# Kernel tuning notes

Hardware: AMD Instinct MI355X
Metric: run time of the kernel (lower is better)

## Reference

```python
import jax, jax.numpy as jnp
import numpy as np
from jax import lax

B, S = 2, 1024
T = B * S
HIDDEN, Q_LORA_RANK = 7168, 1536
N_HEADS, HEAD_DIM, ROPE_DIM = 64, 128, 64
INDEX_TOPK = 2048
QUANT_BLOCK = 128
F8_MAX = 448.0  # float8_e4m3fn max
SOFTMAX_SCALE = HEAD_DIM ** -0.5


def quant_dequant_ue8m0(x):
    """Simulate per-128-block fp8(e4m3) quantization with ue8m0 (power-of-2, ceil) scales."""
    shp = x.shape
    xb = x.reshape(shp[:-1] + (shp[-1] // QUANT_BLOCK, QUANT_BLOCK))
    amax = jnp.max(jnp.abs(xb), axis=-1, keepdims=True)
    scale = jnp.exp2(jnp.ceil(jnp.log2(jnp.maximum(amax, 1e-4) / F8_MAX)))
    q = jnp.clip(xb / scale, -F8_MAX, F8_MAX).astype(jnp.float8_e4m3fn).astype(jnp.float32)
    return (q * scale).reshape(shp)


def rope_cos_sin(positions):
    half = ROPE_DIM // 2
    inv_freq = 1.0 / (10000.0 ** (jnp.arange(half, dtype=jnp.float32) * 2.0 / ROPE_DIM))
    ang = positions.astype(jnp.float32)[:, None] * inv_freq[None, :]  # [T, half]
    return jnp.cos(ang), jnp.sin(ang)


def apply_rope(x, cos, sin):
    half = x.shape[-1] // 2
    x1, x2 = x[..., :half], x[..., half:]
    return jnp.concatenate([x1 * cos - x2 * sin, x1 * sin + x2 * cos], axis=-1)


def setup_inputs() -> dict:
    key = jax.random.key(0)
    k0, k1, k2, k3, k4 = jax.random.split(key, 5)
    std = 0.02
    hidden_states = jax.random.normal(k0, (T, HIDDEN), jnp.float32)
    q_lora = jax.random.normal(k1, (T, Q_LORA_RANK), jnp.float32)
    wq_b = jax.random.normal(k2, (N_HEADS * HEAD_DIM, Q_LORA_RANK), jnp.float32) * std
    wk = jax.random.normal(k3, (HEAD_DIM, HIDDEN), jnp.float32) * std
    k_norm_w = jnp.ones((HEAD_DIM,), jnp.float32)
    k_norm_b = jnp.zeros((HEAD_DIM,), jnp.float32)
    w_proj = jax.random.normal(k4, (N_HEADS, HIDDEN), jnp.float32) * std
    positions = jnp.tile(jnp.arange(S, dtype=jnp.int32), B)  # local position within each sequence
    seq_lens = jnp.full((B,), S, dtype=jnp.int32)
    return {"hidden_states": hidden_states, "q_lora": q_lora, "wq_b": wq_b, "wk": wk,
            "k_norm_w": k_norm_w, "k_norm_b": k_norm_b, "w_proj": w_proj,
            "positions": positions, "seq_lens": seq_lens}


def reference(hidden_states, q_lora, wq_b, wk, k_norm_w, k_norm_b, w_proj, positions, seq_lens):
    # --- projections ---
    q = (q_lora @ wq_b.T).reshape(T, N_HEADS, HEAD_DIM)
    k = hidden_states @ wk.T  # [T, HEAD_DIM]
    # k_norm: LayerNorm(head_dim, eps=1e-6) in fp32
    mu = jnp.mean(k, axis=-1, keepdims=True)
    kc = k - mu
    k = kc * lax.rsqrt(jnp.mean(kc * kc, axis=-1, keepdims=True) + 1e-6) * k_norm_w + k_norm_b
    # --- RoPE on first ROPE_DIM dims of q (per head) and k ---
    cos, sin = rope_cos_sin(positions)
    q = jnp.concatenate([apply_rope(q[..., :ROPE_DIM], cos[:, None, :], sin[:, None, :]),
                         q[..., ROPE_DIM:]], axis=-1)
    k = jnp.concatenate([apply_rope(k[..., :ROPE_DIM], cos, sin), k[..., ROPE_DIM:]], axis=-1)
    # --- fp8 ue8m0 quant-dequant (simulates q_fp8 / per_token_quant_and_transform) ---
    q = quant_dequant_ue8m0(q)
    k = quant_dequant_ue8m0(k)
    # --- head weights (weights_proj, head-count and softmax scaling folded in) ---
    weights = (hidden_states @ w_proj.T) * (N_HEADS ** -0.5) * SOFTMAX_SCALE  # [T, H]
    # --- variable-length causal bounds (compute_cu_seqlen_kv_bounds_nocache) ---
    cu = jnp.concatenate([jnp.zeros((1,), jnp.int32), jnp.cumsum(seq_lens).astype(jnp.int32)])
    batch_ids = jnp.repeat(jnp.arange(seq_lens.shape[0], dtype=jnp.int32), seq_lens,
                           total_repeat_length=T)
    ks_ = cu[batch_ids]                                   # start of each token's KV window
    local_pos = jnp.arange(T, dtype=jnp.int32) - ks_
    ke_ = ks_ + local_pos + 1                             # exclusive end (causal)
    pos_n = jnp.arange(T, dtype=jnp.int32)
    mask = (pos_n[None, :] >= ks_[:, None]) & (pos_n[None, :] < ke_[:, None])  # [T, T]
    # --- fp8_mqa_logits: logits[m,n] = sum_h w[m,h] * relu(q[m,h] . k[n]) ---
    qh = jnp.transpose(q, (1, 0, 2))  # [H, T, D]
    wh = weights.T                    # [H, T]
    def step(acc, hw):
        qh_i, w_i = hw
        return acc + jax.nn.relu(qh_i @ k.T) * w_i[:, None], None
    logits, _ = lax.scan(step, jnp.zeros((T, T), jnp.float32), (qh, wh))
    logits = jnp.where(mask, logits, -jnp.inf)
    # --- top-k selection + local-index remap ---
    k_take = min(INDEX_TOPK, T)
    _, idx = lax.top_k(logits, k_take)
    local = idx - ks_[:, None]
    valid = (local >= 0) & (idx < ke_[:, None])
    topk_indices = jnp.where(valid, local, -1).astype(jnp.int32)
    return logits, topk_indices
```

## Files before the change

### kernel.cpp

```cpp
#include <hip/hip_runtime.h>
#include <math.h>
#include <stdint.h>

#define T_TOK 2048
#define HIDDEN 7168
#define RANK 1536
#define NH 64
#define HD 128
#define NQ (NH*HD)
#define RH 32
#define KSPLIT 8
#define KCHUNK (HIDDEN/KSPLIT)
#define NKW 192

#define MASK_VAL (-3.0e38f)

typedef short bf16x8 __attribute__((ext_vector_type(8)));
typedef float f32x4  __attribute__((ext_vector_type(4)));

#define GLL16(src, dst) __builtin_amdgcn_global_load_lds( \
    (const __attribute__((address_space(1))) void*)(src), \
    (__attribute__((address_space(3))) void*)(dst), 16, 0, 0)

__device__ __forceinline__ float qd_e4m3(float x){
  float ax = fabsf(x);
  float s = (x < 0.f) ? -1.f : 1.f;
  float q;
  if (ax < 0.015625f) {
    q = rintf(ax * 512.f) * 0.001953125f;
  } else {
    int e; (void)frexpf(ax, &e);
    float quant = ldexpf(1.f, e - 4);
    q = rintf(ax / quant) * quant;
  }
  return s * q;
}

__device__ __forceinline__ float ue8m0_scale(float amax){
  float y = fmaxf(amax, 1e-4f) / 448.f;
  int e; float m = frexpf(y, &e);
  int ce = (m == 0.5f) ? (e - 1) : e;
  return ldexpf(1.f, ce);
}

__device__ __forceinline__ unsigned short f2bf_rne(float x){
  unsigned int u = __float_as_uint(x);
  unsigned int r = u + 0x7FFFu + ((u >> 16) & 1u);
  return (unsigned short)(r >> 16);
}

__device__ __forceinline__ void split_bf16(float x, unsigned short& hi, unsigned short& lo){
  unsigned int u = __float_as_uint(x);
  hi = (unsigned short)(u >> 16);
  float xh = __uint_as_float(u & 0xFFFF0000u);
  lo = f2bf_rne(x - xh);
}

__global__ void kt_cossin(const int* __restrict__ pos, float* __restrict__ cost,
                          float* __restrict__ sint){
  int idx = blockIdx.x*256 + threadIdx.x;
  if (idx >= T_TOK*RH) return;
  int t = idx >> 5, j = idx & 31;
  float ex = (float)(2*j) / 64.0f;
  float p10 = (float)pow(10000.0, (double)ex);
  float invf = 1.0f / p10;
  float ang = (float)pos[t] * invf;
  cost[idx] = (float)cos((double)ang);
  sint[idx] = (float)sin((double)ang);
}

__global__ __launch_bounds__(256) void kw_split(const float* __restrict__ Wk,
                                                const float* __restrict__ Wp,
                                                unsigned short* __restrict__ Bh,
                                                unsigned short* __restrict__ Bl){
  int idx = blockIdx.x*256 + threadIdx.x;
  int e0 = idx*8;
  if (e0 >= NKW*HIDDEN) return;
  int n = e0 / HIDDEN, k = e0 - n*HIDDEN;
  const float* src = (n < HD) ? (Wk + (size_t)n*HIDDEN + k) : (Wp + (size_t)(n-HD)*HIDDEN + k);
  float4 a0 = *(const float4*)src;
  float4 a1 = *(const float4*)(src+4);
  float f[8] = {a0.x,a0.y,a0.z,a0.w,a1.x,a1.y,a1.z,a1.w};
  unsigned short h[8], l[8];
  #pragma unroll
  for (int i=0;i<8;i++) split_bf16(f[i], h[i], l[i]);
  *(uint4*)(Bh + e0) = *(const uint4*)h;
  *(uint4*)(Bl + e0) = *(const uint4*)l;
}

__global__ __launch_bounds__(256) void kb3(const float* __restrict__ H,
                                           const unsigned short* __restrict__ Bhg,
                                           const unsigned short* __restrict__ Blg,
                                           float* __restrict__ P){
  __shared__ unsigned short Ah[64*32], Al[64*32], Bh[NKW*32], Bl[NKW*32];
  int ks = blockIdx.x, m0 = blockIdx.y*64, k0 = ks*KCHUNK;
  int tid = threadIdx.x, lane = tid & 63;
  int w = tid >> 6, wr = w >> 1, wc = w & 1;
  int ar = tid >> 2, ac = (tid & 3)*8;
  const float* Arow = H + (size_t)(m0+ar)*HIDDEN + k0 + ac;
  int awb = (ar*64 + ac*2) ^ (((ar>>1)&3)<<4);
  f32x4 acc[2][6];
  #pragma unroll
  for (int i=0;i<2;i++)
    #pragma unroll
    for (int j=0;j<6;j++)
      #pragma unroll
      for (int r=0;r<4;r++) acc[i][j][r] = 0.f;

  for (int kb = 0; kb < KCHUNK; kb += 32){
    float4 a0 = *(const float4*)(Arow + kb);
    float4 a1 = *(const float4*)(Arow + kb + 4);
    __syncthreads();
    {
      float f[8] = {a0.x,a0.y,a0.z,a0.w,a1.x,a1.y,a1.z,a1.w};
      unsigned short h[8], l[8];
      #pragma unroll
      for (int i=0;i<8;i++) split_bf16(f[i], h[i], l[i]);
      *(uint4*)((char*)Ah + awb) = *(const uint4*)h;
      *(uint4*)((char*)Al + awb) = *(const uint4*)l;
    }
    #pragma unroll
    for (int i=0;i<3;i++){
      int ch = w + 4*i;
      int o = ch*1024 + lane*16;
      int row = o >> 6;
      int cb = (o & 63) ^ (((row>>1)&3)<<4);
      size_t srcoff = (size_t)row*HIDDEN + k0 + kb + (cb>>1);
      GLL16(Bhg + srcoff, (char*)Bh + ch*1024);
      GLL16(Blg + srcoff, (char*)Bl + ch*1024);
    }
    __syncthreads();
    bf16x8 ah[2], alr[2], bh[6], bl[6];
    #pragma unroll
    for (int mf=0;mf<2;mf++){
      int rl = wr*32 + mf*16 + (lane&15);
      int ad = (rl*64 + ((lane>>4)*16)) ^ (((rl>>1)&3)<<4);
      ah[mf]  = *(const bf16x8*)((const char*)Ah + ad);
      alr[mf] = *(const bf16x8*)((const char*)Al + ad);
    }
    #pragma unroll
    for (int nf=0;nf<6;nf++){
      int jl = wc*96 + nf*16 + (lane&15);
      int ad = (jl*64 + ((lane>>4)*16)) ^ (((jl>>1)&3)<<4);
      bh[nf] = *(const bf16x8*)((const char*)Bh + ad);
      bl[nf] = *(const bf16x8*)((const char*)Bl + ad);
    }
    #pragma unroll
    for (int mf=0;mf<2;mf++)
      #pragma unroll
      for (int nf=0;nf<6;nf++){
        acc[mf][nf] = __builtin_amdgcn_mfma_f32_16x16x32_bf16(ah[mf],  bh[nf], acc[mf][nf], 0,0,0);
        acc[mf][nf] = __builtin_amdgcn_mfma_f32_16x16x32_bf16(alr[mf], bh[nf], acc[mf][nf], 0,0,0);
        acc[mf][nf] = __builtin_amdgcn_mfma_f32_16x16x32_bf16(ah[mf],  bl[nf], acc[mf][nf], 0,0,0);
      }
  }
  #pragma unroll
  for (int mf=0;mf<2;mf++)
    #pragma unroll
    for (int r=0;r<4;r++){
      int t = m0 + wr*32 + mf*16 + (lane>>4)*4 + r;
      #pragma unroll
      for (int nf=0;nf<6;nf++){
        int n = wc*96 + nf*16 + (lane&15);
        P[((size_t)ks*T_TOK + t)*NKW + n] = acc[mf][nf][r];
      }
    }
}

__global__ __launch_bounds__(128) void kc2(const float* __restrict__ P,
                                           const float* __restrict__ knw,
                                           const float* __restrict__ knb,
                                           const float* __restrict__ cost,
                                           const float* __restrict__ sint,
                                           unsigned short* __restrict__ k16,
                                           float* __restrict__ abuf){
  __shared__ float sh[128];
  __shared__ float red[128];
  int t = blockIdx.x, d = threadIdx.x;
  float v = 0.f;
  #pragma unroll
  for (int s=0;s<KSPLIT;s++) v += P[((size_t)s*T_TOK + t)*NKW + d];
  if (d < NH){
    float wv = 0.f;
    #pragma unroll
    for (int s=0;s<KSPLIT;s++) wv += P[((size_t)s*T_TOK + t)*NKW + HD + d];
    wv = wv * 0.125f;
    wv = wv * 0.08838834764831845f;
    abuf[(size_t)t*NH + d] = wv;
  }
  red[d] = v; __syncthreads();
  for (int s=64;s>0;s>>=1){ if (d<s) red[d] += red[d+s]; __syncthreads(); }
  float mu = red[0] * (1.0f/128.0f); __syncthreads();
  float kc = v - mu;
  red[d] = kc*kc; __syncthreads();
  for (int s=64;s>0;s>>=1){ if (d<s) red[d] += red[d+s]; __syncthreads(); }
  float var = red[0] * (1.0f/128.0f); __syncthreads();
  float rs = 1.0f / sqrtf(var + 1e-6f);
  float nv = ((kc * rs) * knw[d]) + knb[d];
  sh[d] = nv; __syncthreads();
  float rv;
  if (d < RH)            rv = sh[d]*cost[t*RH + d]      - sh[d+RH]*sint[t*RH + d];
  else if (d < 2*RH)     rv = sh[d-RH]*sint[t*RH + d-RH] + sh[d]*cost[t*RH + d-RH];
  else                   rv = nv;
  red[d] = fabsf(rv); __syncthreads();
  for (int s=64;s>0;s>>=1){ if (d<s) red[d] = fmaxf(red[d], red[d+s]); __syncthreads(); }
  float scale = ue8m0_scale(red[0]);
  k16[(size_t)t*HD + d] = f2bf_rne(qd_e4m3(rv / scale) * scale);
}

__global__ __launch_bounds__(256,2) void ka2(const float* __restrict__ A,
                                             const float* __restrict__ B,
                                             const float* __restrict__ cost,
                                             const float* __restrict__ sint,
                                             unsigned short* __restrict__ q16){
  __shared__ unsigned short Ah[128*32], Al[128*32], Bh[128*32], Bl[128*32];
  __shared__ float amx[128][2];
  int n0 = blockIdx.x*128, m0 = blockIdx.y*128;
  int tid = threadIdx.x, lane = tid & 63;
  int w = tid >> 6, wr = w >> 1, wc = w & 1;
  int row = tid >> 1, half = tid & 1;
  const float* Arow = A + (size_t)(m0+row)*RANK + half*16;
  const float* Brow = B + (size_t)(n0+row)*RANK + half*16;
  int sw = ((row >> 1) & 3) << 4;
  int wb0 = row*64 + half*32;
  f32x4 acc[4][4];
  #pragma unroll
  for (int i=0;i<4;i++)
    #pragma unroll
    for (int j=0;j<4;j++)
      #pragma unroll
      for (int r=0;r<4;r++) acc[i][j][r] = 0.f;

  for (int kb = 0; kb < RANK; kb += 32){
    float4 av4[4], bv4[4];
    #pragma unroll
    for (int c=0;c<4;c++) av4[c] = *(const float4*)(Arow + kb + 4*c);
    #pragma unroll
    for (int c=0;c<4;c++) bv4[c] = *(const float4*)(Brow + kb + 4*c);
    __syncthreads();
    {
      unsigned short h[16], l[16];
      const float* f = (const float*)av4;
      #pragma unroll
      for (int i=0;i<16;i++) split_bf16(f[i], h[i], l[i]);
      *(uint4*)((char*)Ah + ((wb0   )^sw)) = *(const uint4*)&h[0];
      *(uint4*)((char*)Ah + ((wb0+16)^sw)) = *(const uint4*)&h[8];
      *(uint4*)((char*)Al + ((wb0   )^sw)) = *(const uint4*)&l[0];
      *(uint4*)((char*)Al + ((wb0+16)^sw)) = *(const uint4*)&l[8];
      const float* g = (const float*)bv4;
      #pragma unroll
      for (int i=0;i<16;i++) split_bf16(g[i], h[i], l[i]);
      *(uint4*)((char*)Bh + ((wb0   )^sw)) = *(const uint4*)&h[0];
      *(uint4*)((char*)Bh + ((wb0+16)^sw)) = *(const uint4*)&h[8];
      *(uint4*)((char*)Bl + ((wb0   )^sw)) = *(const uint4*)&l[0];
      *(uint4*)((char*)Bl + ((wb0+16)^sw)) = *(const uint4*)&l[8];
    }
    __syncthreads();
    bf16x8 ah[4], bh[4], tmp[4];
    #pragma unroll
    for (int mf=0;mf<4;mf++){
      int rl = wr*64 + mf*16 + (lane&15);
      int ad = (rl*64 + ((lane>>4)*16)) ^ ((((rl>>1)&3))<<4);
      ah[mf] = *(const bf16x8*)((const char*)Ah + ad);
    }
    #pragma unroll
    for (int nf=0;nf<4;nf++){
      int rl = wc*64 + nf*16 + (lane&15);
      int ad = (rl*64 + ((lane>>4)*16)) ^ ((((rl>>1)&3))<<4);
      bh[nf] = *(const bf16x8*)((const char*)Bh + ad);
    }
    #pragma unroll
    for (int mf=0;mf<4;mf++)
      #pragma unroll
      for (int nf=0;nf<4;nf++)
        acc[mf][nf] = __builtin_amdgcn_mfma_f32_16x16x32_bf16(ah[mf], bh[nf], acc[mf][nf], 0,0,0);
    #pragma unroll
    for (int mf=0;mf<4;mf++){
      int rl = wr*64 + mf*16 + (lane&15);
      int ad = (rl*64 + ((lane>>4)*16)) ^ ((((rl>>1)&3))<<4);
      tmp[mf] = *(const bf16x8*)((const char*)Al + ad);
    }
    #pragma unroll
    for (int mf=0;mf<4;mf++)
      #pragma unroll
      for (int nf=0;nf<4;nf++)
        acc[mf][nf] = __builtin_amdgcn_mfma_f32_16x16x32_bf16(tmp[mf], bh[nf], acc[mf][nf], 0,0,0);
    #pragma unroll
    for (int nf=0;nf<4;nf++){
      int rl = wc*64 + nf*16 + (lane&15);
      int ad = (rl*64 + ((lane>>4)*16)) ^ ((((rl>>1)&3))<<4);
      tmp[nf] = *(const bf16x8*)((const char*)Bl + ad);
    }
    #pragma unroll
    for (int mf=0;mf<4;mf++)
      #pragma unroll
      for (int nf=0;nf<4;nf++)
        acc[mf][nf] = __builtin_amdgcn_mfma_f32_16x16x32_bf16(ah[mf], tmp[nf], acc[mf][nf], 0,0,0);
  }

  if (wc == 0){
    #pragma unroll
    for (int mf=0;mf<4;mf++)
      #pragma unroll
      for (int r=0;r<4;r++){
        int t = m0 + wr*64 + mf*16 + (lane>>4)*4 + r;
        #pragma unroll
        for (int nf=0;nf<2;nf++){
          int d0 = nf*16 + (lane&15);
          float c = cost[t*RH + d0], s = sint[t*RH + d0];
          float x1 = acc[mf][nf][r], x2 = acc[mf][nf+2][r];
          acc[mf][nf][r]   = __fsub_rn(__fmul_rn(x1,c), __fmul_rn(x2,s));
          acc[mf][nf+2][r] = __fadd_rn(__fmul_rn(x1,s), __fmul_rn(x2,c));
        }
      }
  }
  float pm[16];
  #pragma unroll
  for (int mf=0;mf<4;mf++)
    #pragma unroll
    for (int r=0;r<4;r++){
      float m1 = fmaxf(fabsf(acc[mf][0][r]), fabsf(acc[mf][1][r]));
      float m2 = fmaxf(fabsf(acc[mf][2][r]), fabsf(acc[mf][3][r]));
      pm[mf*4+r] = fmaxf(m1, m2);
    }
  #pragma unroll
  for (int msk=1; msk<16; msk<<=1)
    #pragma unroll
    for (int i=0;i<16;i++) pm[i] = fmaxf(pm[i], __shfl_xor(pm[i], msk, 16));
  if ((lane & 15) == 0){
    #pragma unroll
    for (int mf=0;mf<4;mf++)
      #pragma unroll
      for (int r=0;r<4;r++)
        amx[wr*64 + mf*16 + (lane>>4)*4 + r][wc] = pm[mf*4+r];
  }
  __syncthreads();
  #pragma unroll
  for (int mf=0;mf<4;mf++)
    #pragma unroll
    for (int r=0;r<4;r++){
      int rl = wr*64 + mf*16 + (lane>>4)*4 + r;
      int t = m0 + rl;
      float scl = ue8m0_scale(fmaxf(amx[rl][0], amx[rl][1]));
      #pragma unroll
      for (int nf=0;nf<4;nf++){
        float v = acc[mf][nf][r];
        float qv = qd_e4m3(v / scl) * scl;
        q16[(size_t)t*NQ + n0 + wc*64 + nf*16 + (lane&15)] = f2bf_rne(qv);
      }
    }
}

__global__ __launch_bounds__(256,2) void ke2(const unsigned short* __restrict__ q16,
                                             const unsigned short* __restrict__ k16,
                                             const float* __restrict__ W,
                                             const int* __restrict__ seq,
                                             float* __restrict__ out){
  __shared__ unsigned short Kt[128*128];
  __shared__ unsigned short Qt[2][64*128];
  __shared__ float Wl[64*64];
  int j0 = blockIdx.x*128, t0 = blockIdx.y*64;
  int tid = threadIdx.x;
  int s0 = seq[0];
  int ks0 = (t0 < s0) ? 0 : s0;
  if (j0 > t0 + 63 || j0 + 127 < ks0){
    int tl = tid >> 2, c0 = (tid & 3) * 32;
    float4 m4 = make_float4(MASK_VAL, MASK_VAL, MASK_VAL, MASK_VAL);
    float* rowp = out + (size_t)(t0+tl)*T_TOK + j0 + c0;
    #pragma unroll
    for (int c=0;c<32;c+=4) *(float4*)(rowp + c) = m4;
    return;
  }
  int lane = tid & 63, w = tid >> 6, wt = w >> 1, wj = w & 1;
  #pragma unroll
  for (int is=0; is<8; ++is){
    int o = is*4096 + w*1024 + lane*16;
    int row = o >> 8;
    int os = o ^ ((row & 7) << 4);
    int col = (os & 255) >> 1;
    GLL16(k16 + (size_t)(j0 + row)*HD + col, (char*)Kt + is*4096 + w*1024);
  }
  {
    int tl = tid >> 2, h0 = (tid & 3) * 16;
    float wv[16];
    #pragma unroll
    for (int c=0;c<4;c++) *(float4*)&wv[4*c] = *(const float4*)(W + (size_t)(t0+tl)*NH + h0 + 4*c);
    #pragma unroll
    for (int i=0;i<16;i++) Wl[(h0+i)*64 + tl] = wv[i];
  }
  #pragma unroll
  for (int is=0; is<4; ++is){
    int o = is*4096 + w*1024 + lane*16;
    int row = o >> 8;
    int os = o ^ ((row & 7) << 4);
    int col = (os & 255) >> 1;
    GLL16(q16 + (size_t)(t0 + row)*NQ + 0*HD + col, (char*)&Qt[0][0] + is*4096 + w*1024);
  }
  __syncthreads();
  bf16x8 bk[4][4];
  #pragma unroll
  for (int jf=0;jf<4;jf++){
    int jl = wj*64 + jf*16 + (lane&15);
    int sz = (jl & 7) << 4;
    #pragma unroll
    for (int kf=0;kf<4;kf++)
      bk[jf][kf] = *(const bf16x8*)((const char*)Kt + ((jl*256 + kf*64 + ((lane>>4)*16)) ^ sz));
  }
  bool skip = (j0 + wj*64 > t0 + wt*32 + 31) || (j0 + wj*64 + 63 < ks0);
  f32x4 acc[2][4];
  #pragma unroll
  for (int a=0;a<2;a++)
    #pragma unroll
    for (int b=0;b<4;b++)
      #pragma unroll
      for (int r=0;r<4;r++) acc[a][b][r] = 0.f;

  for (int h = 0; h < NH; ++h){
    if (h < NH-1){
      char* dst = (char*)&Qt[(h+1)&1][0];
      #pragma unroll
      for (int is=0; is<4; ++is){
        int o = is*4096 + w*1024 + lane*16;
        int row = o >> 8;
        int os = o ^ ((row & 7) << 4);
        int col = (os & 255) >> 1;
        GLL16(q16 + (size_t)(t0 + row)*NQ + (size_t)(h+1)*HD + col, dst + is*4096 + w*1024);
      }
    }
    if (!skip){
      const char* qb = (const char*)&Qt[h&1][0];
      bf16x8 aq[2][4];
      #pragma unroll
      for (int tf=0;tf<2;tf++){
        int tl = wt*32 + tf*16 + (lane&15);
        int sz = (tl & 7) << 4;
        #pragma unroll
        for (int kf=0;kf<4;kf++)
          aq[tf][kf] = *(const bf16x8*)(qb + ((tl*256 + kf*64 + ((lane>>4)*16)) ^ sz));
      }
      f32x4 pp[2][4];
      #pragma unroll
      for (int a=0;a<2;a++)
        #pragma unroll
        for (int b=0;b<4;b++)
          #pragma unroll
          for (int r=0;r<4;r++) pp[a][b][r] = 0.f;
      #pragma unroll
      for (int kf=0;kf<4;kf++)
        #pragma unroll
        for (int tf=0;tf<2;tf++)
          #pragma unroll
          for (int jf=0;jf<4;jf++)
            pp[tf][jf] = __builtin_amdgcn_mfma_f32_16x16x32_bf16(aq[tf][kf], bk[jf][kf], pp[tf][jf], 0,0,0);
      #pragma unroll
      for (int tf=0;tf<2;tf++)
        #pragma unroll
        for (int r=0;r<4;r++){
          float wv = Wl[h*64 + wt*32 + tf*16 + (lane>>4)*4 + r];
          #pragma unroll
          for (int jf=0;jf<4;jf++)
            acc[tf][jf][r] = fmaf(wv, fmaxf(pp[tf][jf][r], 0.f), acc[tf][jf][r]);
        }
    }
    __syncthreads();
  }
  #pragma unroll
  for (int tf=0;tf<2;tf++)
    #pragma unroll
    for (int r=0;r<4;r++){
      int t = t0 + wt*32 + tf*16 + (lane>>4)*4 + r;
      #pragma unroll
      for (int jf=0;jf<4;jf++){
        int j = j0 + wj*64 + jf*16 + (lane&15);
        bool ok = (j >= ks0) && (j <= t);
        out[(size_t)t*T_TOK + j] = ok ? acc[tf][jf][r] : MASK_VAL;
      }
    }
}

__global__ __launch_bounds__(256) void kf_topk(const float* __restrict__ logits,
                                               const int* __restrict__ seq,
                                               float* __restrict__ outIdx){
  __shared__ unsigned long long keys[1024];
  int t = blockIdx.x, tid = threadIdx.x;
  int s0 = seq[0];
  int ks = (t < s0) ? 0 : s0;
  int nv = t - ks + 1;
  for (int i = tid; i < 1024; i += 256){
    unsigned long long key = 0ull;
    if (i < nv){
      float v = logits[(size_t)t*T_TOK + ks + i];
      unsigned int b = __float_as_uint(v);
      unsigned int ov = (b & 0x80000000u) ? ~b : (b | 0x80000000u);
      key = ((unsigned long long)ov << 32) | (unsigned long long)(0x7FFFFFFFu - (unsigned)i);
    }
    keys[i] = key;
  }
  for (int size = 2; size <= 1024; size <<= 1){
    for (int stride = size >> 1; stride > 0; stride >>= 1){
      __syncthreads();
      for (int i = tid; i < 1024; i += 256){
        int p = i ^ stride;
        if (p > i){
          bool up = (i & size) == 0;
          unsigned long long a = keys[i], b2 = keys[p];
          if (up ? (a < b2) : (a > b2)){ keys[i] = b2; keys[p] = a; }
        }
      }
    }
  }
  __syncthreads();
  for (int p = tid; p < T_TOK; p += 256){
    float o = -1.0f;
    if (p < nv){
      unsigned int low = (unsigned int)(keys[p] & 0xFFFFFFFFull);
      o = (float)(int)(0x7FFFFFFFu - low);
    }
    outIdx[(size_t)t*T_TOK + p] = o;
  }
}

extern "C" void kernel_launch(void* const* d_in, const int* in_sizes, int n_in,
                              void* d_out, int out_size, void* d_ws, size_t ws_size,
                              hipStream_t stream){
  const float* hidden  = (const float*)d_in[0];
  const float* q_lora  = (const float*)d_in[1];
  const float* wq_b    = (const float*)d_in[2];
  const float* wk      = (const float*)d_in[3];
  const float* knw     = (const float*)d_in[4];
  const float* knb     = (const float*)d_in[5];
  const float* wproj   = (const float*)d_in[6];
  const int* positions = (const int*)d_in[7];
  const int* seq       = (const int*)d_in[8];

  char* ws = (char*)d_ws;
  unsigned short* q16 = (unsigned short*)ws;              ws += (size_t)T_TOK*NQ*2;
  float* P = (float*)ws;                                  ws += (size_t)KSPLIT*T_TOK*NKW*4;
  unsigned short* Whg = (unsigned short*)ws;              ws += (size_t)NKW*HIDDEN*2;
  unsigned short* Wlg = (unsigned short*)ws;              ws += (size_t)NKW*HIDDEN*2;
  unsigned short* k16 = (unsigned short*)ws;              ws += (size_t)T_TOK*HD*2;
  float* abuf = (float*)ws;                               ws += (size_t)T_TOK*NH*4;
  float* cost = (float*)ws;                               ws += (size_t)T_TOK*RH*4;
  float* sint = (float*)ws;                               ws += (size_t)T_TOK*RH*4;

  float* logits = (float*)d_out;
  float* topk   = logits + (size_t)T_TOK*T_TOK;

  kt_cossin<<<(T_TOK*RH)/256, 256, 0, stream>>>(positions, cost, sint);
  kw_split <<<(NKW*HIDDEN/8 + 255)/256, 256, 0, stream>>>(wk, wproj, Whg, Wlg);
  kb3      <<<dim3(KSPLIT, T_TOK/64), 256, 0, stream>>>(hidden, Whg, Wlg, P);
  kc2      <<<T_TOK, 128, 0, stream>>>(P, knw, knb, cost, sint, k16, abuf);
  ka2      <<<dim3(NQ/128, T_TOK/128), 256, 0, stream>>>(q_lora, wq_b, cost, sint, q16);
  ke2      <<<dim3(T_TOK/128, T_TOK/64), 256, 0, stream>>>(q16, k16, abuf, seq, logits);
  kf_topk  <<<T_TOK, 256, 0, stream>>>(logits, seq, topk);
}
```

Baseline: 348.8 us.

## Merge Q and K/weight projection GEMMs into one heterogeneous launch

```diff
diff --git a/kernel.cpp b/kernel.cpp
--- a/kernel.cpp
+++ b/kernel.cpp
@@ -88,83 +88,236 @@
   *(uint4*)(Bl + e0) = *(const uint4*)l;
 }
 
-__global__ __launch_bounds__(256) void kb3(const float* __restrict__ H,
-                                           const unsigned short* __restrict__ Bhg,
-                                           const unsigned short* __restrict__ Blg,
-                                           float* __restrict__ P){
-  __shared__ unsigned short Ah[64*32], Al[64*32], Bh[NKW*32], Bl[NKW*32];
-  int ks = blockIdx.x, m0 = blockIdx.y*64, k0 = ks*KCHUNK;
+__global__ __launch_bounds__(256,2) void kfat(const float* __restrict__ A,
+                                              const float* __restrict__ B,
+                                              const float* __restrict__ cost,
+                                              const float* __restrict__ sint,
+                                              unsigned short* __restrict__ q16,
+                                              const float* __restrict__ H,
+                                              const unsigned short* __restrict__ Bhg,
+                                              const unsigned short* __restrict__ Blg,
+                                              float* __restrict__ P){
+  __shared__ char smem[33792] __attribute__((aligned(16)));
+  int bid = blockIdx.x;
   int tid = threadIdx.x, lane = tid & 63;
-  int w = tid >> 6, wr = w >> 1, wc = w & 1;
-  int ar = tid >> 2, ac = (tid & 3)*8;
-  const float* Arow = H + (size_t)(m0+ar)*HIDDEN + k0 + ac;
-  int awb = (ar*64 + ac*2) ^ (((ar>>1)&3)<<4);
-  f32x4 acc[2][6];
-  #pragma unroll
-  for (int i=0;i<2;i++)
-    #pragma unroll
-    for (int j=0;j<6;j++)
-      #pragma unroll
-      for (int r=0;r<4;r++) acc[i][j][r] = 0.f;
-
-  for (int kb = 0; kb < KCHUNK; kb += 32){
-    float4 a0 = *(const float4*)(Arow + kb);
-    float4 a1 = *(const float4*)(Arow + kb + 4);
+
+  if (bid < 1024){
+    unsigned short* Ah = (unsigned short*)smem;
+    unsigned short* Al = Ah + 128*32;
+    unsigned short* Bh = Al + 128*32;
+    unsigned short* Bl = Bh + 128*32;
+    float (*amx)[2] = (float(*)[2])(smem + 32768);
+    int n0 = (bid & 63)*128, m0 = (bid >> 6)*128;
+    int w = tid >> 6, wr = w >> 1, wc = w & 1;
+    int row = tid >> 1, half = tid & 1;
+    const float* Arow = A + (size_t)(m0+row)*RANK + half*16;
+    const float* Brow = B + (size_t)(n0+row)*RANK + half*16;
+    int sw = ((row >> 1) & 3) << 4;
+    int wb0 = row*64 + half*32;
+    f32x4 acc[4][4];
+    #pragma unroll
+    for (int i=0;i<4;i++)
+      #pragma unroll
+      for (int j=0;j<4;j++)
+        #pragma unroll
+        for (int r=0;r<4;r++) acc[i][j][r] = 0.f;
+
+    for (int kb = 0; kb < RANK; kb += 32){
+      float4 av4[4], bv4[4];
+      #pragma unroll
+      for (int c=0;c<4;c++) av4[c] = *(const float4*)(Arow + kb + 4*c);
+      #pragma unroll
+      for (int c=0;c<4;c++) bv4[c] = *(const float4*)(Brow + kb + 4*c);
+      __syncthreads();
+      {
+        unsigned short h[16], l[16];
+        const float* f = (const float*)av4;
+        #pragma unroll
+        for (int i=0;i<16;i++) split_bf16(f[i], h[i], l[i]);
+        *(uint4*)((char*)Ah + ((wb0   )^sw)) = *(const uint4*)&h[0];
+        *(uint4*)((char*)Ah + ((wb0+16)^sw)) = *(const uint4*)&h[8];
+        *(uint4*)((char*)Al + ((wb0   )^sw)) = *(const uint4*)&l[0];
+        *(uint4*)((char*)Al + ((wb0+16)^sw)) = *(const uint4*)&l[8];
+        const float* g = (const float*)bv4;
+        #pragma unroll
+        for (int i=0;i<16;i++) split_bf16(g[i], h[i], l[i]);
+        *(uint4*)((char*)Bh + ((wb0   )^sw)) = *(const uint4*)&h[0];
+        *(uint4*)((char*)Bh + ((wb0+16)^sw)) = *(const uint4*)&h[8];
+        *(uint4*)((char*)Bl + ((wb0   )^sw)) = *(const uint4*)&l[0];
+        *(uint4*)((char*)Bl + ((wb0+16)^sw)) = *(const uint4*)&l[8];
+      }
+      __syncthreads();
+      bf16x8 ah[4], bh[4], tmp[4];
+      #pragma unroll
+      for (int mf=0;mf<4;mf++){
+        int rl = wr*64 + mf*16 + (lane&15);
+        int ad = (rl*64 + ((lane>>4)*16)) ^ ((((rl>>1)&3))<<4);
+        ah[mf] = *(const bf16x8*)((const char*)Ah + ad);
+      }
+      #pragma unroll
+      for (int nf=0;nf<4;nf++){
+        int rl = wc*64 + nf*16 + (lane&15);
+        int ad = (rl*64 + ((lane>>4)*16)) ^ ((((rl>>1)&3))<<4);
+        bh[nf] = *(const bf16x8*)((const char*)Bh + ad);
+      }
+      #pragma unroll
+      for (int mf=0;mf<4;mf++)
+        #pragma unroll
+        for (int nf=0;nf<4;nf++)
+          acc[mf][nf] = __builtin_amdgcn_mfma_f32_16x16x32_bf16(ah[mf], bh[nf], acc[mf][nf], 0,0,0);
+      #pragma unroll
+      for (int mf=0;mf<4;mf++){
+        int rl = wr*64 + mf*16 + (lane&15);
+        int ad = (rl*64 + ((lane>>4)*16)) ^ ((((rl>>1)&3))<<4);
+        tmp[mf] = *(const bf16x8*)((const char*)Al + ad);
+      }
+      #pragma unroll
+      for (int mf=0;mf<4;mf++)
+        #pragma unroll
+        for (int nf=0;nf<4;nf++)
+          acc[mf][nf] = __builtin_amdgcn_mfma_f32_16x16x32_bf16(tmp[mf], bh[nf], acc[mf][nf], 0,0,0);
+      #pragma unroll
+      for (int nf=0;nf<4;nf++){
+        int rl = wc*64 + nf*16 + (lane&15);
+        int ad = (rl*64 + ((lane>>4)*16)) ^ ((((rl>>1)&3))<<4);
+        tmp[nf] = *(const bf16x8*)((const char*)Bl + ad);
+      }
+      #pragma unroll
+      for (int mf=0;mf<4;mf++)
+        #pragma unroll
+        for (int nf=0;nf<4;nf++)
+          acc[mf][nf] = __builtin_amdgcn_mfma_f32_16x16x32_bf16(ah[mf], tmp[nf], acc[mf][nf], 0,0,0);
+    }
+
+    if (wc == 0){
+      #pragma unroll
+      for (int mf=0;mf<4;mf++)
+        #pragma unroll
+        for (int r=0;r<4;r++){
+          int t = m0 + wr*64 + mf*16 + (lane>>4)*4 + r;
+          #pragma unroll
+          for (int nf=0;nf<2;nf++){
+            int d0 = nf*16 + (lane&15);
+            float c = cost[t*RH + d0], s = sint[t*RH + d0];
+            float x1 = acc[mf][nf][r], x2 = acc[mf][nf+2][r];
+            acc[mf][nf][r]   = __fsub_rn(__fmul_rn(x1,c), __fmul_rn(x2,s));
+            acc[mf][nf+2][r] = __fadd_rn(__fmul_rn(x1,s), __fmul_rn(x2,c));
+          }
+        }
+    }
+    float pm[16];
+    #pragma unroll
+    for (int mf=0;mf<4;mf++)
+      #pragma unroll
+      for (int r=0;r<4;r++){
+        float m1 = fmaxf(fabsf(acc[mf][0][r]), fabsf(acc[mf][1][r]));
+        float m2 = fmaxf(fabsf(acc[mf][2][r]), fabsf(acc[mf][3][r]));
+        pm[mf*4+r] = fmaxf(m1, m2);
+      }
+    #pragma unroll
+    for (int msk=1; msk<16; msk<<=1)
+      #pragma unroll
+      for (int i=0;i<16;i++) pm[i] = fmaxf(pm[i], __shfl_xor(pm[i], msk, 16));
+    if ((lane & 15) == 0){
+      #pragma unroll
+      for (int mf=0;mf<4;mf++)
+        #pragma unroll
+        for (int r=0;r<4;r++)
+          amx[wr*64 + mf*16 + (lane>>4)*4 + r][wc] = pm[mf*4+r];
+    }
     __syncthreads();
-    {
-      float f[8] = {a0.x,a0.y,a0.z,a0.w,a1.x,a1.y,a1.z,a1.w};
-      unsigned short h[8], l[8];
-      #pragma unroll
-      for (int i=0;i<8;i++) split_bf16(f[i], h[i], l[i]);
-      *(uint4*)((char*)Ah + awb) = *(const uint4*)h;
-      *(uint4*)((char*)Al + awb) = *(const uint4*)l;
-    }
-    #pragma unroll
-    for (int i=0;i<3;i++){
-      int ch = w + 4*i;
-      int o = ch*1024 + lane*16;
-      int row = o >> 6;
-      int cb = (o & 63) ^ (((row>>1)&3)<<4);
-      size_t srcoff = (size_t)row*HIDDEN + k0 + kb + (cb>>1);
-      GLL16(Bhg + srcoff, (char*)Bh + ch*1024);
-      GLL16(Blg + srcoff, (char*)Bl + ch*1024);
-    }
-    __syncthreads();
-    bf16x8 ah[2], alr[2], bh[6], bl[6];
-    #pragma unroll
-    for (int mf=0;mf<2;mf++){
-      int rl = wr*32 + mf*16 + (lane&15);
-      int ad = (rl*64 + ((lane>>4)*16)) ^ (((rl>>1)&3)<<4);
-      ah[mf]  = *(const bf16x8*)((const char*)Ah + ad);
-      alr[mf] = *(const bf16x8*)((const char*)Al + ad);
-    }
-    #pragma unroll
-    for (int nf=0;nf<6;nf++){
-      int jl = wc*96 + nf*16 + (lane&15);
-      int ad = (jl*64 + ((lane>>4)*16)) ^ (((jl>>1)&3)<<4);
-      bh[nf] = *(const bf16x8*)((const char*)Bh + ad);
-      bl[nf] = *(const bf16x8*)((const char*)Bl + ad);
+    #pragma unroll
+    for (int mf=0;mf<4;mf++)
+      #pragma unroll
+      for (int r=0;r<4;r++){
+        int rl = wr*64 + mf*16 + (lane>>4)*4 + r;
+        int t = m0 + rl;
+        float scl = ue8m0_scale(fmaxf(amx[rl][0], amx[rl][1]));
+        #pragma unroll
+        for (int nf=0;nf<4;nf++){
+          float v = acc[mf][nf][r];
+          float qv = qd_e4m3(v / scl) * scl;
+          q16[(size_t)t*NQ + n0 + wc*64 + nf*16 + (lane&15)] = f2bf_rne(qv);
+        }
+      }
+  } else {
+    unsigned short* Ah = (unsigned short*)smem;
+    unsigned short* Al = Ah + 64*32;
+    unsigned short* Bh = Al + 64*32;
+    unsigned short* Bl = Bh + NKW*32;
+    int b2 = bid - 1024;
+    int ks = b2 & 7, m0 = (b2 >> 3)*64, k0 = ks*KCHUNK;
+    int w = tid >> 6, wr = w >> 1, wc = w & 1;
+    int ar = tid >> 2, ac = (tid & 3)*8;
+    const float* Arow = H + (size_t)(m0+ar)*HIDDEN + k0 + ac;
+    int awb = (ar*64 + ac*2) ^ (((ar>>1)&3)<<4);
+    f32x4 acc[2][6];
+    #pragma unroll
+    for (int i=0;i<2;i++)
+      #pragma unroll
+      for (int j=0;j<6;j++)
+        #pragma unroll
+        for (int r=0;r<4;r++) acc[i][j][r] = 0.f;
+
+    for (int kb = 0; kb < KCHUNK; kb += 32){
+      float4 a0 = *(const float4*)(Arow + kb);
+      float4 a1 = *(const float4*)(Arow + kb + 4);
+      __syncthreads();
+      {
+        float f[8] = {a0.x,a0.y,a0.z,a0.w,a1.x,a1.y,a1.z,a1.w};
+        unsigned short h[8], l[8];
+        #pragma unroll
+        for (int i=0;i<8;i++) split_bf16(f[i], h[i], l[i]);
+        *(uint4*)((char*)Ah + awb) = *(const uint4*)h;
+        *(uint4*)((char*)Al + awb) = *(const uint4*)l;
+      }
+      #pragma unroll
+      for (int i=0;i<3;i++){
+        int ch = w + 4*i;
+        int o = ch*1024 + lane*16;
+        int row = o >> 6;
+        int cb = (o & 63) ^ (((row>>1)&3)<<4);
+        size_t srcoff = (size_t)row*HIDDEN + k0 + kb + (cb>>1);
+        GLL16(Bhg + srcoff, (char*)Bh + ch*1024);
+        GLL16(Blg + srcoff, (char*)Bl + ch*1024);
+      }
+      __syncthreads();
+      bf16x8 ah[2], alr[2], bh[6], bl[6];
+      #pragma unroll
+      for (int mf=0;mf<2;mf++){
+        int rl = wr*32 + mf*16 + (lane&15);
+        int ad = (rl*64 + ((lane>>4)*16)) ^ (((rl>>1)&3)<<4);
+        ah[mf]  = *(const bf16x8*)((const char*)Ah + ad);
+        alr[mf] = *(const bf16x8*)((const char*)Al + ad);
+      }
+      #pragma unroll
+      for (int nf=0;nf<6;nf++){
+        int jl = wc*96 + nf*16 + (lane&15);
+        int ad = (jl*64 + ((lane>>4)*16)) ^ (((jl>>1)&3)<<4);
+        bh[nf] = *(const bf16x8*)((const char*)Bh + ad);
+        bl[nf] = *(const bf16x8*)((const char*)Bl + ad);
+      }
+      #pragma unroll
+      for (int mf=0;mf<2;mf++)
+        #pragma unroll
+        for (int nf=0;nf<6;nf++){
+          acc[mf][nf] = __builtin_amdgcn_mfma_f32_16x16x32_bf16(ah[mf],  bh[nf], acc[mf][nf], 0,0,0);
+          acc[mf][nf] = __builtin_amdgcn_mfma_f32_16x16x32_bf16(alr[mf], bh[nf], acc[mf][nf], 0,0,0);
+          acc[mf][nf] = __builtin_amdgcn_mfma_f32_16x16x32_bf16(ah[mf],  bl[nf], acc[mf][nf], 0,0,0);
+        }
     }
     #pragma unroll
     for (int mf=0;mf<2;mf++)
       #pragma unroll
-      for (int nf=0;nf<6;nf++){
-        acc[mf][nf] = __builtin_amdgcn_mfma_f32_16x16x32_bf16(ah[mf],  bh[nf], acc[mf][nf], 0,0,0);
-        acc[mf][nf] = __builtin_amdgcn_mfma_f32_16x16x32_bf16(alr[mf], bh[nf], acc[mf][nf], 0,0,0);
-        acc[mf][nf] = __builtin_amdgcn_mfma_f32_16x16x32_bf16(ah[mf],  bl[nf], acc[mf][nf], 0,0,0);
-      }
-  }
-  #pragma unroll
-  for (int mf=0;mf<2;mf++)
-    #pragma unroll
-    for (int r=0;r<4;r++){
-      int t = m0 + wr*32 + mf*16 + (lane>>4)*4 + r;
-      #pragma unroll
-      for (int nf=0;nf<6;nf++){
-        int n = wc*96 + nf*16 + (lane&15);
-        P[((size_t)ks*T_TOK + t)*NKW + n] = acc[mf][nf][r];
-      }
-    }
+      for (int r=0;r<4;r++){
+        int t = m0 + wr*32 + mf*16 + (lane>>4)*4 + r;
+        #pragma unroll
+        for (int nf=0;nf<6;nf++){
+          int n = wc*96 + nf*16 + (lane&15);
+          P[((size_t)ks*T_TOK + t)*NKW + n] = acc[mf][nf][r];
+        }
+      }
+  }
 }
 
 __global__ __launch_bounds__(128) void kc2(const float* __restrict__ P,
@@ -208,149 +361,6 @@
   k16[(size_t)t*HD + d] = f2bf_rne(qd_e4m3(rv / scale) * scale);
 }
 
-__global__ __launch_bounds__(256,2) void ka2(const float* __restrict__ A,
-                                             const float* __restrict__ B,
-                                             const float* __restrict__ cost,
-                                             const float* __restrict__ sint,
-                                             unsigned short* __restrict__ q16){
-  __shared__ unsigned short Ah[128*32], Al[128*32], Bh[128*32], Bl[128*32];
-  __shared__ float amx[128][2];
-  int n0 = blockIdx.x*128, m0 = blockIdx.y*128;
-  int tid = threadIdx.x, lane = tid & 63;
-  int w = tid >> 6, wr = w >> 1, wc = w & 1;
-  int row = tid >> 1, half = tid & 1;
-  const float* Arow = A + (size_t)(m0+row)*RANK + half*16;
-  const float* Brow = B + (size_t)(n0+row)*RANK + half*16;
-  int sw = ((row >> 1) & 3) << 4;
-  int wb0 = row*64 + half*32;
-  f32x4 acc[4][4];
-  #pragma unroll
-  for (int i=0;i<4;i++)
-    #pragma unroll
-    for (int j=0;j<4;j++)
-      #pragma unroll
-      for (int r=0;r<4;r++) acc[i][j][r] = 0.f;
-
-  for (int kb = 0; kb < RANK; kb += 32){
-    float4 av4[4], bv4[4];
-    #pragma unroll
-    for (int c=0;c<4;c++) av4[c] = *(const float4*)(Arow + kb + 4*c);
-    #pragma unroll
-    for (int c=0;c<4;c++) bv4[c] = *(const float4*)(Brow + kb + 4*c);
-    __syncthreads();
-    {
-      unsigned short h[16], l[16];
-      const float* f = (const float*)av4;
-      #pragma unroll
-      for (int i=0;i<16;i++) split_bf16(f[i], h[i], l[i]);
-      *(uint4*)((char*)Ah + ((wb0   )^sw)) = *(const uint4*)&h[0];
-      *(uint4*)((char*)Ah + ((wb0+16)^sw)) = *(const uint4*)&h[8];
-      *(uint4*)((char*)Al + ((wb0   )^sw)) = *(const uint4*)&l[0];
-      *(uint4*)((char*)Al + ((wb0+16)^sw)) = *(const uint4*)&l[8];
-      const float* g = (const float*)bv4;
-      #pragma unroll
-      for (int i=0;i<16;i++) split_bf16(g[i], h[i], l[i]);
-      *(uint4*)((char*)Bh + ((wb0   )^sw)) = *(const uint4*)&h[0];
-      *(uint4*)((char*)Bh + ((wb0+16)^sw)) = *(const uint4*)&h[8];
-      *(uint4*)((char*)Bl + ((wb0   )^sw)) = *(const uint4*)&l[0];
-      *(uint4*)((char*)Bl + ((wb0+16)^sw)) = *(const uint4*)&l[8];
-    }
-    __syncthreads();
-    bf16x8 ah[4], bh[4], tmp[4];
-    #pragma unroll
-    for (int mf=0;mf<4;mf++){
-      int rl = wr*64 + mf*16 + (lane&15);
-      int ad = (rl*64 + ((lane>>4)*16)) ^ ((((rl>>1)&3))<<4);
-      ah[mf] = *(const bf16x8*)((const char*)Ah + ad);
-    }
-    #pragma unroll
-    for (int nf=0;nf<4;nf++){
-      int rl = wc*64 + nf*16 + (lane&15);
-      int ad = (rl*64 + ((lane>>4)*16)) ^ ((((rl>>1)&3))<<4);
-      bh[nf] = *(const bf16x8*)((const char*)Bh + ad);
-    }
-    #pragma unroll
-    for (int mf=0;mf<4;mf++)
-      #pragma unroll
-      for (int nf=0;nf<4;nf++)
-        acc[mf][nf] = __builtin_amdgcn_mfma_f32_16x16x32_bf16(ah[mf], bh[nf], acc[mf][nf], 0,0,0);
-    #pragma unroll
-    for (int mf=0;mf<4;mf++){
-      int rl = wr*64 + mf*16 + (lane&15);
-      int ad = (rl*64 + ((lane>>4)*16)) ^ ((((rl>>1)&3))<<4);
-      tmp[mf] = *(const bf16x8*)((const char*)Al + ad);
-    }
-    #pragma unroll
-    for (int mf=0;mf<4;mf++)
-      #pragma unroll
-      for (int nf=0;nf<4;nf++)
-        acc[mf][nf] = __builtin_amdgcn_mfma_f32_16x16x32_bf16(tmp[mf], bh[nf], acc[mf][nf], 0,0,0);
-    #pragma unroll
-    for (int nf=0;nf<4;nf++){
-      int rl = wc*64 + nf*16 + (lane&15);
-      int ad = (rl*64 + ((lane>>4)*16)) ^ ((((rl>>1)&3))<<4);
-      tmp[nf] = *(const bf16x8*)((const char*)Bl + ad);
-    }
-    #pragma unroll
-    for (int mf=0;mf<4;mf++)
-      #pragma unroll
-      for (int nf=0;nf<4;nf++)
-        acc[mf][nf] = __builtin_amdgcn_mfma_f32_16x16x32_bf16(ah[mf], tmp[nf], acc[mf][nf], 0,0,0);
-  }
-
-  if (wc == 0){
-    #pragma unroll
-    for (int mf=0;mf<4;mf++)
-      #pragma unroll
-      for (int r=0;r<4;r++){
-        int t = m0 + wr*64 + mf*16 + (lane>>4)*4 + r;
-        #pragma unroll
-        for (int nf=0;nf<2;nf++){
-          int d0 = nf*16 + (lane&15);
-          float c = cost[t*RH + d0], s = sint[t*RH + d0];
-          float x1 = acc[mf][nf][r], x2 = acc[mf][nf+2][r];
-          acc[mf][nf][r]   = __fsub_rn(__fmul_rn(x1,c), __fmul_rn(x2,s));
-          acc[mf][nf+2][r] = __fadd_rn(__fmul_rn(x1,s), __fmul_rn(x2,c));
-        }
-      }
-  }
-  float pm[16];
-  #pragma unroll
-  for (int mf=0;mf<4;mf++)
-    #pragma unroll
-    for (int r=0;r<4;r++){
-      float m1 = fmaxf(fabsf(acc[mf][0][r]), fabsf(acc[mf][1][r]));
-      float m2 = fmaxf(fabsf(acc[mf][2][r]), fabsf(acc[mf][3][r]));
-      pm[mf*4+r] = fmaxf(m1, m2);
-    }
-  #pragma unroll
-  for (int msk=1; msk<16; msk<<=1)
-    #pragma unroll
-    for (int i=0;i<16;i++) pm[i] = fmaxf(pm[i], __shfl_xor(pm[i], msk, 16));
-  if ((lane & 15) == 0){
-    #pragma unroll
-    for (int mf=0;mf<4;mf++)
-      #pragma unroll
-      for (int r=0;r<4;r++)
-        amx[wr*64 + mf*16 + (lane>>4)*4 + r][wc] = pm[mf*4+r];
-  }
-  __syncthreads();
-  #pragma unroll
-  for (int mf=0;mf<4;mf++)
-    #pragma unroll
-    for (int r=0;r<4;r++){
-      int rl = wr*64 + mf*16 + (lane>>4)*4 + r;
-      int t = m0 + rl;
-      float scl = ue8m0_scale(fmaxf(amx[rl][0], amx[rl][1]));
-      #pragma unroll
-      for (int nf=0;nf<4;nf++){
-        float v = acc[mf][nf][r];
-        float qv = qd_e4m3(v / scl) * scl;
-        q16[(size_t)t*NQ + n0 + wc*64 + nf*16 + (lane&15)] = f2bf_rne(qv);
-      }
-    }
-}
-
 __global__ __launch_bounds__(256,2) void ke2(const unsigned short* __restrict__ q16,
                                              const unsigned short* __restrict__ k16,
                                              const float* __restrict__ W,
@@ -548,9 +558,9 @@
 
   kt_cossin<<<(T_TOK*RH)/256, 256, 0, stream>>>(positions, cost, sint);
   kw_split <<<(NKW*HIDDEN/8 + 255)/256, 256, 0, stream>>>(wk, wproj, Whg, Wlg);
-  kb3      <<<dim3(KSPLIT, T_TOK/64), 256, 0, stream>>>(hidden, Whg, Wlg, P);
+  kfat     <<<1280, 256, 0, stream>>>(q_lora, wq_b, cost, sint, q16,
+                                      hidden, Whg, Wlg, P);
   kc2      <<<T_TOK, 128, 0, stream>>>(P, knw, knb, cost, sint, k16, abuf);
-  ka2      <<<dim3(NQ/128, T_TOK/128), 256, 0, stream>>>(q_lora, wq_b, cost, sint, q16);
   ke2      <<<dim3(T_TOK/128, T_TOK/64), 256, 0, stream>>>(q16, k16, abuf, seq, logits);
   kf_topk  <<<T_TOK, 256, 0, stream>>>(logits, seq, topk);
 }
```

New measurement: 318.2 us. 8.8% less time.
